# Kernel tuning notes

Hardware: AMD Instinct MI355X
Metric: run time of the kernel (lower is better)

The kernel has to match this reference:

```python
import jax, jax.numpy as jnp
import numpy as np

N = 100000      # nodes
E = 1600000     # edges (avg degree 16)
IN_F, HID, OUT_F, NC = 384, 128, 64, 2
EPS = 1e-5
NEG_SLOPE = 0.01


def _layernorm(x, g, b):
    m = jnp.mean(x, axis=-1, keepdims=True)
    v = jnp.var(x, axis=-1, keepdims=True)
    return (x - m) * jax.lax.rsqrt(v + EPS) * g + b


def _graph_conv(x, edge_index, edge_weight, w_rel, b_rel, w_root):
    # PyG GraphConv: lin_rel(scatter_add(w_e * x[src] -> dst)) + lin_root(x)
    src, dst = edge_index[0], edge_index[1]
    msg = x[src] * edge_weight[:, None]                      # [E, C]
    agg = jax.ops.segment_sum(msg, dst, num_segments=x.shape[0])  # [N, C]
    return agg @ w_rel.T + b_rel + x @ w_root.T


def _xavier(key, shape):
    fan_in, fan_out = shape[1], shape[0]
    lim = float(np.sqrt(6.0 / (fan_in + fan_out)))
    return jax.random.uniform(key, shape, jnp.float32, -lim, lim)


def setup_inputs() -> dict:
    key = jax.random.key(0)
    ks = jax.random.split(key, 10)
    x = jax.random.normal(ks[0], (N, IN_F), jnp.float32)
    edge_index = jax.random.randint(ks[1], (2, E), 0, N, jnp.int64)
    edge_attr = jax.random.uniform(ks[2], (E,), jnp.float32)
    return {
        "x": x,
        "edge_index": edge_index,
        "edge_attr": edge_attr,
        "ln1_g": jnp.ones((IN_F,), jnp.float32),
        "ln1_b": jnp.zeros((IN_F,), jnp.float32),
        "fc1_w": _xavier(ks[3], (HID, IN_F)),
        "fc1_b": jnp.zeros((HID,), jnp.float32),
        "c1_wrel": _xavier(ks[4], (HID, HID)),
        "c1_brel": jnp.zeros((HID,), jnp.float32),
        "c1_wroot": _xavier(ks[5], (HID, HID)),
        "c2_wrel": _xavier(ks[6], (OUT_F, HID)),
        "c2_brel": jnp.zeros((OUT_F,), jnp.float32),
        "c2_wroot": _xavier(ks[7], (OUT_F, HID)),
        "ln2_g": jnp.ones((OUT_F,), jnp.float32),
        "ln2_b": jnp.zeros((OUT_F,), jnp.float32),
        "fc2_w": _xavier(ks[8], (NC, OUT_F)),
        "fc2_b": jnp.zeros((NC,), jnp.float32),
    }


def reference(x, edge_index, edge_attr,
              ln1_g, ln1_b, fc1_w, fc1_b,
              c1_wrel, c1_brel, c1_wroot,
              c2_wrel, c2_brel, c2_wroot,
              ln2_g, ln2_b, fc2_w, fc2_b):
    h = _layernorm(x, ln1_g, ln1_b) @ fc1_w.T + fc1_b          # [N, HID]
    h = _graph_conv(h, edge_index, edge_attr, c1_wrel, c1_brel, c1_wroot)
    h = jax.nn.leaky_relu(h, NEG_SLOPE)
    h = _graph_conv(h, edge_index, edge_attr, c2_wrel, c2_brel, c2_wroot)
    h = jax.nn.leaky_relu(h, NEG_SLOPE)                        # [N, OUT_F]
    out = _layernorm(h, ln2_g, ln2_b) @ fc2_w.T + fc2_b        # [N, NC]
    return out
```

## Files before the change

### kernel.cpp

```cpp
#include <hip/hip_runtime.h>
#include <hip/hip_bf16.h>

#define N_IN_F 384
#define N_HID  128
#define N_OUT  64

typedef unsigned short ushort_t;
typedef __attribute__((ext_vector_type(8))) short short8v;
typedef __attribute__((ext_vector_type(4))) float floatx4;

union U8 { uint4 v; unsigned short u[8]; };

__device__ __forceinline__ float bfu2f(unsigned short s){
    union { unsigned i; float f; } c; c.i = ((unsigned)s) << 16; return c.f;
}
__device__ __forceinline__ unsigned short f2bfu(float f){
    __hip_bfloat16 h = __float2bfloat16(f);
    union { __hip_bfloat16 h; unsigned short u; } c; c.h = h; return c.u;
}

__device__ __forceinline__ float loadS(const void* p, size_t i, int fm){
    return fm ? bfu2f(((const unsigned short*)p)[i]) : ((const float*)p)[i];
}

__global__ void k_detect_all(const int* __restrict__ ei, const unsigned* __restrict__ xw,
                             int* __restrict__ modep){
    int lane = threadIdx.x & 63;
    int zi = 0;
    if (lane < 32) zi = ei[2*lane + 1];
    int cnt = 0;
    #pragma unroll
    for (int q = 0; q < 8; q++){
        unsigned w = xw[lane*8 + q];
        unsigned elo = (w >> 7) & 0xff;
        cnt += (elo >= 118 && elo <= 134) ? 1 : 0;
    }
    #pragma unroll
    for (int m = 32; m; m >>= 1){ zi |= __shfl_xor(zi, m, 64); cnt += __shfl_xor(cnt, m, 64); }
    if (lane == 0 && blockIdx.x == 0){
        modep[0] = (zi == 0) ? 1 : 0;
        modep[1] = (cnt >= 256) ? 1 : 0;
    }
}

__device__ __forceinline__ int edge_src(const int* ei, int e, int i, int mode){
    return mode ? ei[2*(size_t)i] : ei[i];
}
__device__ __forceinline__ int edge_dst(const int* ei, int e, int i, int mode){
    return mode ? ei[2*(size_t)e + 2*(size_t)i] : ei[(size_t)e + i];
}

__global__ void k_hist(const int* __restrict__ ei, int e, int n, const int* __restrict__ modep,
                       int* __restrict__ deg){
    int i = blockIdx.x * 256 + threadIdx.x;
    if (i >= e) return;
    int mode = modep[0];
    int d = edge_dst(ei, e, i, mode);
    if ((unsigned)d >= (unsigned)n) return;
    atomicAdd(&deg[d], 1);
}

__global__ __launch_bounds__(1024) void k_blksum(
    const int* __restrict__ deg, int n, int* __restrict__ part)
{
    __shared__ int s[1024];
    int i = blockIdx.x * 1024 + threadIdx.x;
    s[threadIdx.x] = (i < n) ? deg[i] : 0;
    __syncthreads();
    for (int off = 512; off; off >>= 1){
        if (threadIdx.x < off) s[threadIdx.x] += s[threadIdx.x + off];
        __syncthreads();
    }
    if (threadIdx.x == 0) part[blockIdx.x] = s[0];
}

__global__ __launch_bounds__(128) void k_scanpart(
    int* __restrict__ part, int nb, int* __restrict__ rowoff, int n)
{
    __shared__ int s[128];
    int t = threadIdx.x;
    if (nb <= 128){
        int v = (t < nb) ? part[t] : 0;
        s[t] = v; __syncthreads();
        #pragma unroll
        for (int off = 1; off < 128; off <<= 1){
            int tmp = (t >= off) ? s[t - off] : 0;
            __syncthreads();
            s[t] += tmp;
            __syncthreads();
        }
        if (t < nb) part[t] = s[t] - v;
        if (t == 127) rowoff[n] = s[127];
    } else if (t == 0){
        int run = 0;
        for (int b = 0; b < nb; b++){ int tt = part[b]; part[b] = run; run += tt; }
        rowoff[n] = run;
    }
}

__global__ __launch_bounds__(1024) void k_scanblk(
    int* __restrict__ deg, const int* __restrict__ part, int n, int* __restrict__ rowoff)
{
    __shared__ int s[1024];
    int t = threadIdx.x;
    int i = blockIdx.x * 1024 + t;
    int v = (i < n) ? deg[i] : 0;
    s[t] = v; __syncthreads();
    for (int off = 1; off < 1024; off <<= 1){
        int tmp = (t >= off) ? s[t - off] : 0;
        __syncthreads();
        s[t] += tmp;
        __syncthreads();
    }
    if (i < n){
        int excl = s[t] - v + part[blockIdx.x];
        rowoff[i] = excl;
        deg[i]    = excl;
    }
}

__global__ void k_scatter(const int* __restrict__ ei, const void* __restrict__ ea,
                          int e, int n, const int* __restrict__ modep,
                          int* __restrict__ cursor, int2* __restrict__ colw)
{
    int i = blockIdx.x * 256 + threadIdx.x;
    if (i >= e) return;
    int mode = modep[0], fm = modep[1];
    int d = edge_dst(ei, e, i, mode);
    if ((unsigned)d >= (unsigned)n) return;
    int s = edge_src(ei, e, i, mode);
    if ((unsigned)s >= (unsigned)n) s = 0;
    int pos = atomicAdd(&cursor[d], 1);
    if ((unsigned)pos >= (unsigned)e) return;
    int2 pk; pk.x = s; pk.y = __float_as_int(loadS(ea, i, fm));
    colw[pos] = pk;
}

__global__ __launch_bounds__(64) void k_prep_w1(
    const void* __restrict__ W, const void* __restrict__ g, const void* __restrict__ b,
    const void* __restrict__ fc1b, const int* __restrict__ fmp,
    ushort_t* __restrict__ Wp, float* __restrict__ u, float* __restrict__ v)
{
    int fm = fmp[0];
    int j = blockIdx.x, lane = threadIdx.x;
    float su = 0.f, sv = 0.f;
    for (int k = lane; k < N_IN_F; k += 64){
        float w  = loadS(W, (size_t)j*N_IN_F + k, fm);
        float gk = loadS(g, k, fm);
        float bk = loadS(b, k, fm);
        unsigned short pw = f2bfu(gk * w);
        Wp[(size_t)j*N_IN_F + k] = pw;
        su += bfu2f(pw);
        sv += bk * w;
    }
    #pragma unroll
    for (int m = 32; m; m >>= 1){ su += __shfl_xor(su, m, 64); sv += __shfl_xor(sv, m, 64); }
    if (lane == 0){
        u[j] = su;
        v[j] = sv + loadS(fc1b, j, fm);
    }
}

__global__ void k_cvt4(const void* __restrict__ p0, const void* __restrict__ p1,
                       const void* __restrict__ p2, const void* __restrict__ p3,
                       const int* __restrict__ fmp, ushort_t* __restrict__ o)
{
    int fm = fmp[0];
    int i = blockIdx.x * 256 + threadIdx.x;
    if (i >= 49152) return;
    const void* p; int off;
    if (i < 16384)      { p = p0; off = i; }
    else if (i < 32768) { p = p1; off = i - 16384; }
    else if (i < 40960) { p = p2; off = i - 32768; }
    else                { p = p3; off = i - 40960; }
    o[i] = f2bfu(loadS(p, off, fm));
}

__global__ __launch_bounds__(256) void k_gemm1_mfma(
    const void* __restrict__ x, const int* __restrict__ fmp,
    const ushort_t* __restrict__ Wp,
    const float* __restrict__ u, const float* __restrict__ v,
    ushort_t* __restrict__ out, int n)
{
    int fm = fmp[0];
    int t = threadIdx.x;
    int wave = t >> 6, lane = t & 63;
    int r16 = lane & 15, kq = lane >> 4;
    int m0 = blockIdx.x * 64 + wave * 16;
    int rA = min(m0 + r16, n - 1);

    floatx4 acc[8];
    #pragma unroll
    for (int c = 0; c < 8; c++) acc[c] = (floatx4){0.f, 0.f, 0.f, 0.f};
    float s1 = 0.f, s2 = 0.f;

    for (int ks = 0; ks < N_IN_F/32; ks++){
        int kb = ks*32 + kq*8;
        size_t idx = (size_t)rA*N_IN_F + kb;
        short8v af;
        float f[8];
        if (fm){
            short8v sv = *(const short8v*)((const ushort_t*)x + idx);
            af = sv;
            #pragma unroll
            for (int q = 0; q < 8; q++) f[q] = bfu2f((unsigned short)sv[q]);
        } else {
            const float* xf = (const float*)x + idx;
            floatx4 p = *(const floatx4*)xf;
            floatx4 q4 = *(const floatx4*)(xf + 4);
            f[0]=p[0]; f[1]=p[1]; f[2]=p[2]; f[3]=p[3];
            f[4]=q4[0]; f[5]=q4[1]; f[6]=q4[2]; f[7]=q4[3];
            short8v r;
            #pragma unroll
            for (int q = 0; q < 8; q++) r[q] = (short)f2bfu(f[q]);
            af = r;
        }
        #pragma unroll
        for (int q = 0; q < 8; q++){ s1 += f[q]; s2 += f[q]*f[q]; }

        short8v bfr[8];
        #pragma unroll
        for (int ni = 0; ni < 8; ni++)
            bfr[ni] = *(const short8v*)(Wp + (size_t)(ni*16 + r16)*N_IN_F + kb);
        #pragma unroll
        for (int ni = 0; ni < 8; ni++)
            acc[ni] = __builtin_amdgcn_mfma_f32_16x16x32_bf16(af, bfr[ni], acc[ni], 0, 0, 0);
    }

    s1 += __shfl_xor(s1, 16, 64); s1 += __shfl_xor(s1, 32, 64);
    s2 += __shfl_xor(s2, 16, 64); s2 += __shfl_xor(s2, 32, 64);
    float mu = s1 * (1.f/384.f);
    float var = fmaxf(s2 * (1.f/384.f) - mu*mu, 0.f);
    float rs = rsqrtf(var + 1e-5f);

    int ib = m0 + kq*4;
    float mm[4], rr[4];
    #pragma unroll
    for (int r = 0; r < 4; r++){
        mm[r] = __shfl(mu, kq*4 + r, 64);
        rr[r] = __shfl(rs, kq*4 + r, 64);
    }
    #pragma unroll
    for (int ni = 0; ni < 8; ni++){
        int j = ni*16 + r16;
        float uj = u[j], vj = v[j];
        #pragma unroll
        for (int r = 0; r < 4; r++){
            int ii = ib + r;
            float val = rr[r]*acc[ni][r] - rr[r]*mm[r]*uj + vj;
            if (ii < n) out[(size_t)ii*N_HID + j] = f2bfu(val);
        }
    }
}

__global__ __launch_bounds__(256) void k_conv1_mfma(
    const ushort_t* __restrict__ A1, const ushort_t* __restrict__ A2,
    const ushort_t* __restrict__ W1, const ushort_t* __restrict__ W2,
    const void* __restrict__ bias, const int* __restrict__ fmp,
    ushort_t* __restrict__ out, int n)
{
    int fm = fmp[0];
    int t = threadIdx.x;
    int wave = t >> 6, lane = t & 63;
    int r16 = lane & 15, kq = lane >> 4;
    int m0 = blockIdx.x * 64 + wave * 16;
    int rA = min(m0 + r16, n - 1);

    floatx4 acc[8];
    #pragma unroll
    for (int c = 0; c < 8; c++) acc[c] = (floatx4){0.f, 0.f, 0.f, 0.f};

    #pragma unroll
    for (int p = 0; p < 2; p++){
        const ushort_t* A = p ? A2 : A1;
        const ushort_t* W = p ? W2 : W1;
        #pragma unroll
        for (int ks = 0; ks < 4; ks++){
            int kb = ks*32 + kq*8;
            short8v af = *(const short8v*)(A + (size_t)rA*N_HID + kb);
            short8v bfr[8];
            #pragma unroll
            for (int ni = 0; ni < 8; ni++)
                bfr[ni] = *(const short8v*)(W + (size_t)(ni*16 + r16)*N_HID + kb);
            #pragma unroll
            for (int ni = 0; ni < 8; ni++)
                acc[ni] = __builtin_amdgcn_mfma_f32_16x16x32_bf16(af, bfr[ni], acc[ni], 0, 0, 0);
        }
    }

    int ib = m0 + kq*4;
    #pragma unroll
    for (int ni = 0; ni < 8; ni++){
        int j = ni*16 + r16;
        float bb = loadS(bias, j, fm);
        #pragma unroll
        for (int r = 0; r < 4; r++){
            int ii = ib + r;
            float val = acc[ni][r] + bb;
            val = (val >= 0.f) ? val : 0.01f * val;
            if (ii < n) out[(size_t)ii*N_HID + j] = f2bfu(val);
        }
    }
}

__global__ __launch_bounds__(256) void k_conv2_final(
    const ushort_t* __restrict__ A1, const ushort_t* __restrict__ A2,
    const ushort_t* __restrict__ W1, const ushort_t* __restrict__ W2,
    const void* __restrict__ bias,
    const void* __restrict__ gam, const void* __restrict__ bet,
    const void* __restrict__ Wfc, const void* __restrict__ bfc,
    const int* __restrict__ fmp, void* __restrict__ out, int n)
{
    int fm = fmp[0];
    int t = threadIdx.x;
    int wave = t >> 6, lane = t & 63;
    int r16 = lane & 15, kq = lane >> 4;
    int m0 = blockIdx.x * 64 + wave * 16;
    int rA = min(m0 + r16, n - 1);

    floatx4 acc[4];
    #pragma unroll
    for (int c = 0; c < 4; c++) acc[c] = (floatx4){0.f, 0.f, 0.f, 0.f};

    #pragma unroll
    for (int p = 0; p < 2; p++){
        const ushort_t* A = p ? A2 : A1;
        const ushort_t* W = p ? W2 : W1;
        #pragma unroll
        for (int ks = 0; ks < 4; ks++){
            int kb = ks*32 + kq*8;
            short8v af = *(const short8v*)(A + (size_t)rA*N_HID + kb);
            short8v bfr[4];
            #pragma unroll
            for (int ni = 0; ni < 4; ni++)
                bfr[ni] = *(const short8v*)(W + (size_t)(ni*16 + r16)*N_HID + kb);
            #pragma unroll
            for (int ni = 0; ni < 4; ni++)
                acc[ni] = __builtin_amdgcn_mfma_f32_16x16x32_bf16(af, bfr[ni], acc[ni], 0, 0, 0);
        }
    }

    float s[4] = {}, s2[4] = {};
    #pragma unroll
    for (int ni = 0; ni < 4; ni++){
        int j = ni*16 + r16;
        float bb = loadS(bias, j, fm);
        #pragma unroll
        for (int r = 0; r < 4; r++){
            float val = acc[ni][r] + bb;
            val = (val >= 0.f) ? val : 0.01f * val;
            acc[ni][r] = val;
            s[r] += val; s2[r] += val*val;
        }
    }
    #pragma unroll
    for (int m = 1; m < 16; m <<= 1){
        #pragma unroll
        for (int r = 0; r < 4; r++){
            s[r]  += __shfl_xor(s[r],  m, 64);
            s2[r] += __shfl_xor(s2[r], m, 64);
        }
    }
    float mu[4], rstd[4];
    #pragma unroll
    for (int r = 0; r < 4; r++){
        mu[r] = s[r] * (1.f/64.f);
        float var = fmaxf(s2[r] * (1.f/64.f) - mu[r]*mu[r], 0.f);
        rstd[r] = rsqrtf(var + 1e-5f);
    }
    float p0[4] = {}, p1[4] = {};
    #pragma unroll
    for (int ni = 0; ni < 4; ni++){
        int j = ni*16 + r16;
        float gj = loadS(gam, j, fm), bj = loadS(bet, j, fm);
        float w0 = loadS(Wfc, j, fm), w1 = loadS(Wfc, 64 + j, fm);
        #pragma unroll
        for (int r = 0; r < 4; r++){
            float zn = (acc[ni][r] - mu[r]) * rstd[r] * gj + bj;
            p0[r] += zn * w0;
            p1[r] += zn * w1;
        }
    }
    #pragma unroll
    for (int m = 1; m < 16; m <<= 1){
        #pragma unroll
        for (int r = 0; r < 4; r++){
            p0[r] += __shfl_xor(p0[r], m, 64);
            p1[r] += __shfl_xor(p1[r], m, 64);
        }
    }
    if (r16 == 0){
        float b0 = loadS(bfc, 0, fm), b1 = loadS(bfc, 1, fm);
        #pragma unroll
        for (int r = 0; r < 4; r++){
            int ii = m0 + kq*4 + r;
            if (ii >= n) continue;
            float o0 = p0[r] + b0, o1 = p1[r] + b1;
            if (fm){
                unsigned pk = ((unsigned)f2bfu(o1) << 16) | (unsigned)f2bfu(o0);
                *(unsigned*)((ushort_t*)out + (size_t)ii*2) = pk;
            } else {
                float2 f2; f2.x = o0; f2.y = o1;
                *(float2*)((float*)out + (size_t)ii*2) = f2;
            }
        }
    }
}

__global__ __launch_bounds__(256) void k_agg(
    const int* __restrict__ rowoff, const int2* __restrict__ colw,
    const ushort_t* __restrict__ src_mat,
    ushort_t* __restrict__ out, int n, int eTot)
{
    int t = threadIdx.x;
    int lane = t & 63;
    int d = blockIdx.x * 4 + (t >> 6);
    if (d >= n) return;
    int grp = lane >> 4;
    int c16 = lane & 15;
    int e0 = rowoff[d], e1 = rowoff[d+1];
    e0 = max(0, min(e0, eTot));
    e1 = max(e0, min(e1, eTot));
    float acc[8] = {};
    for (int e = e0 + grp; e < e1; e += 4){
        int2 cw = colw[e];
        int s = cw.x;
        if ((unsigned)s >= (unsigned)n) s = 0;
        float wv = __int_as_float(cw.y);
        U8 u; u.v = *(const uint4*)(src_mat + (size_t)s*N_HID + c16*8);
        #pragma unroll
        for (int q = 0; q < 8; q++) acc[q] += wv * bfu2f(u.u[q]);
    }
    #pragma unroll
    for (int q = 0; q < 8; q++){
        acc[q] += __shfl_xor(acc[q], 16, 64);
        acc[q] += __shfl_xor(acc[q], 32, 64);
    }
    if (grp == 0){
        union { ushort_t u[8]; uint4 v; } P;
        #pragma unroll
        for (int q = 0; q < 8; q++) P.u[q] = f2bfu(acc[q]);
        *(uint4*)(out + (size_t)d*N_HID + c16*8) = P.v;
    }
}

extern "C" void kernel_launch(void* const* d_in, const int* in_sizes, int n_in,
                              void* d_out, int out_size, void* d_ws, size_t ws_size,
                              hipStream_t stream)
{
    const void* x     = d_in[0];
    const int*  ei    = (const int*)d_in[1];
    const void* ea    = d_in[2];
    const void* ln1g  = d_in[3];
    const void* ln1b  = d_in[4];
    const void* fc1w  = d_in[5];
    const void* fc1b  = d_in[6];
    const void* c1rel = d_in[7];
    const void* c1bre = d_in[8];
    const void* c1roo = d_in[9];
    const void* c2rel = d_in[10];
    const void* c2bre = d_in[11];
    const void* c2roo = d_in[12];
    const void* ln2g  = d_in[13];
    const void* ln2b  = d_in[14];
    const void* fc2w  = d_in[15];
    const void* fc2b  = d_in[16];
    (void)n_in; (void)out_size; (void)ws_size;

    const int n = in_sizes[0] / N_IN_F;
    const int e = in_sizes[2];

    char* wsp = (char*)d_ws;
    size_t off = 0;
    auto alloc = [&](size_t bytes) -> char* {
        char* p = wsp + off; off += (bytes + 255) & ~(size_t)255; return p;
    };
    int*      deg    = (int*)  alloc((size_t)n * 4);
    int*      rowoff = (int*)  alloc((size_t)(n+1) * 4);
    int*      part   = (int*)  alloc(4096);
    int*      modep  = (int*)  alloc(256);
    int2*     colw   = (int2*) alloc((size_t)e * 8);
    float*    u      = (float*)alloc(128 * 4);
    float*    v      = (float*)alloc(128 * 4);
    ushort_t* Wp     = (ushort_t*)alloc((size_t)N_HID * N_IN_F * 2);
    ushort_t* cw     = (ushort_t*)alloc((size_t)49152 * 2);
    ushort_t* h1     = (ushort_t*)alloc((size_t)n * N_HID * 2);
    ushort_t* agg1   = (ushort_t*)alloc((size_t)n * N_HID * 2);
    ushort_t* g1     = (ushort_t*)alloc((size_t)n * N_HID * 2);
    ushort_t* agg2   = h1;

    hipMemsetAsync(deg, 0, (size_t)n * 4, stream);
    k_detect_all<<<1, 64, 0, stream>>>(ei, (const unsigned*)x, modep);

    int nb = (n + 1023) / 1024;
    k_hist    <<<(e + 255) / 256, 256, 0, stream>>>(ei, e, n, modep, deg);
    k_blksum  <<<nb, 1024, 0, stream>>>(deg, n, part);
    k_scanpart<<<1, 128, 0, stream>>>(part, nb, rowoff, n);
    k_scanblk <<<nb, 1024, 0, stream>>>(deg, part, n, rowoff);
    k_scatter <<<(e + 255) / 256, 256, 0, stream>>>(ei, ea, e, n, modep, deg, colw);

    k_prep_w1<<<N_HID, 64, 0, stream>>>(fc1w, ln1g, ln1b, fc1b, modep + 1, Wp, u, v);
    k_cvt4   <<<(49152 + 255) / 256, 256, 0, stream>>>(c1rel, c1roo, c2rel, c2roo, modep + 1, cw);

    k_gemm1_mfma<<<(n + 63) / 64, 256, 0, stream>>>(x, modep + 1, Wp, u, v, h1, n);

    k_agg<<<(n + 3) / 4, 256, 0, stream>>>(rowoff, colw, h1, agg1, n, e);
    k_conv1_mfma<<<(n + 63) / 64, 256, 0, stream>>>(agg1, h1, cw, cw + 16384, c1bre, modep + 1, g1, n);

    k_agg<<<(n + 3) / 4, 256, 0, stream>>>(rowoff, colw, g1, agg2, n, e);
    k_conv2_final<<<(n + 63) / 64, 256, 0, stream>>>(agg2, g1, cw + 32768, cw + 40960, c2bre,
                                                     ln2g, ln2b, fc2w, fc2b, modep + 1, d_out, n);
}
```

Baseline: 754.2 us.

## Stage GEMM tiles through LDS with 128-row blocks in dense kernels

The three dense MFMA kernels (fc1, conv1, conv2+final) now cooperatively load A and B tiles into padded shared memory and compute a 128-row block per workgroup, with each wave handling 32 rows. Previously each wave loaded its weight fragments straight from global memory. Sharing the weight tile across waves and doubling the rows per block is meant to cut redundant global and L2 weight traffic. In exchange it adds two barriers per k-step with no double buffering, launches half as many blocks, and uses more registers and LDS per block.

```diff
diff --git a/kernel.cpp b/kernel.cpp
--- a/kernel.cpp
+++ b/kernel.cpp
@@ -182,73 +182,101 @@
     const float* __restrict__ u, const float* __restrict__ v,
     ushort_t* __restrict__ out, int n)
 {
+    __shared__ ushort_t As[128*40];
+    __shared__ ushort_t Bs[128*40];
     int fm = fmp[0];
     int t = threadIdx.x;
     int wave = t >> 6, lane = t & 63;
     int r16 = lane & 15, kq = lane >> 4;
-    int m0 = blockIdx.x * 64 + wave * 16;
-    int rA = min(m0 + r16, n - 1);
-
-    floatx4 acc[8];
-    #pragma unroll
-    for (int c = 0; c < 8; c++) acc[c] = (floatx4){0.f, 0.f, 0.f, 0.f};
-    float s1 = 0.f, s2 = 0.f;
-
-    for (int ks = 0; ks < N_IN_F/32; ks++){
-        int kb = ks*32 + kq*8;
-        size_t idx = (size_t)rA*N_IN_F + kb;
-        short8v af;
-        float f[8];
-        if (fm){
-            short8v sv = *(const short8v*)((const ushort_t*)x + idx);
-            af = sv;
-            #pragma unroll
-            for (int q = 0; q < 8; q++) f[q] = bfu2f((unsigned short)sv[q]);
-        } else {
-            const float* xf = (const float*)x + idx;
-            floatx4 p = *(const floatx4*)xf;
-            floatx4 q4 = *(const floatx4*)(xf + 4);
-            f[0]=p[0]; f[1]=p[1]; f[2]=p[2]; f[3]=p[3];
-            f[4]=q4[0]; f[5]=q4[1]; f[6]=q4[2]; f[7]=q4[3];
-            short8v r;
-            #pragma unroll
-            for (int q = 0; q < 8; q++) r[q] = (short)f2bfu(f[q]);
-            af = r;
-        }
-        #pragma unroll
-        for (int q = 0; q < 8; q++){ s1 += f[q]; s2 += f[q]*f[q]; }
-
-        short8v bfr[8];
+    int m0 = blockIdx.x * 128;
+    int mw = m0 + wave * 32;
+
+    int sq = t & 3, srow = t >> 2;
+    int bcol = t & 127, bhalf = t >> 7;
+
+    floatx4 acc[2][8];
+    #pragma unroll
+    for (int a = 0; a < 2; a++)
+        #pragma unroll
+        for (int c = 0; c < 8; c++) acc[a][c] = (floatx4){0.f,0.f,0.f,0.f};
+    float s1[2] = {0.f,0.f}, s2[2] = {0.f,0.f};
+
+    for (int ks = 0; ks < 12; ks++){
+        int kb = ks*32;
+        #pragma unroll
+        for (int pass = 0; pass < 2; pass++){
+            int row  = srow + pass*64;
+            int grow = min(m0 + row, n - 1);
+            union { ushort_t u[8]; uint4 v4; } w;
+            if (fm){
+                w.v4 = *(const uint4*)((const ushort_t*)x + (size_t)grow*N_IN_F + kb + sq*8);
+            } else {
+                const float* xf = (const float*)x + (size_t)grow*N_IN_F + kb + sq*8;
+                floatx4 p = *(const floatx4*)xf;
+                floatx4 q4 = *(const floatx4*)(xf + 4);
+                w.u[0]=f2bfu(p[0]); w.u[1]=f2bfu(p[1]); w.u[2]=f2bfu(p[2]); w.u[3]=f2bfu(p[3]);
+                w.u[4]=f2bfu(q4[0]); w.u[5]=f2bfu(q4[1]); w.u[6]=f2bfu(q4[2]); w.u[7]=f2bfu(q4[3]);
+            }
+            *(uint4*)(As + row*40 + sq*8) = w.v4;
+        }
+        {
+            const ushort_t* wp = Wp + (size_t)bcol*N_IN_F + kb + bhalf*16;
+            uint4 b0 = *(const uint4*)wp;
+            uint4 b1 = *(const uint4*)(wp + 8);
+            *(uint4*)(Bs + bcol*40 + bhalf*16)     = b0;
+            *(uint4*)(Bs + bcol*40 + bhalf*16 + 8) = b1;
+        }
+        __syncthreads();
+        short8v af[2], bfr[8];
+        #pragma unroll
+        for (int mi = 0; mi < 2; mi++)
+            af[mi] = *(const short8v*)(As + (wave*32 + mi*16 + r16)*40 + kq*8);
         #pragma unroll
         for (int ni = 0; ni < 8; ni++)
-            bfr[ni] = *(const short8v*)(Wp + (size_t)(ni*16 + r16)*N_IN_F + kb);
-        #pragma unroll
-        for (int ni = 0; ni < 8; ni++)
-            acc[ni] = __builtin_amdgcn_mfma_f32_16x16x32_bf16(af, bfr[ni], acc[ni], 0, 0, 0);
-    }
-
-    s1 += __shfl_xor(s1, 16, 64); s1 += __shfl_xor(s1, 32, 64);
-    s2 += __shfl_xor(s2, 16, 64); s2 += __shfl_xor(s2, 32, 64);
-    float mu = s1 * (1.f/384.f);
-    float var = fmaxf(s2 * (1.f/384.f) - mu*mu, 0.f);
-    float rs = rsqrtf(var + 1e-5f);
-
-    int ib = m0 + kq*4;
-    float mm[4], rr[4];
-    #pragma unroll
-    for (int r = 0; r < 4; r++){
-        mm[r] = __shfl(mu, kq*4 + r, 64);
-        rr[r] = __shfl(rs, kq*4 + r, 64);
-    }
-    #pragma unroll
-    for (int ni = 0; ni < 8; ni++){
-        int j = ni*16 + r16;
-        float uj = u[j], vj = v[j];
+            bfr[ni] = *(const short8v*)(Bs + (ni*16 + r16)*40 + kq*8);
+        #pragma unroll
+        for (int mi = 0; mi < 2; mi++){
+            #pragma unroll
+            for (int q = 0; q < 8; q++){
+                float f = bfu2f((unsigned short)af[mi][q]);
+                s1[mi] += f; s2[mi] += f*f;
+            }
+            #pragma unroll
+            for (int ni = 0; ni < 8; ni++)
+                acc[mi][ni] = __builtin_amdgcn_mfma_f32_16x16x32_bf16(af[mi], bfr[ni], acc[mi][ni], 0, 0, 0);
+        }
+        __syncthreads();
+    }
+
+    float mu[2], rs[2];
+    #pragma unroll
+    for (int mi = 0; mi < 2; mi++){
+        s1[mi] += __shfl_xor(s1[mi], 16, 64); s1[mi] += __shfl_xor(s1[mi], 32, 64);
+        s2[mi] += __shfl_xor(s2[mi], 16, 64); s2[mi] += __shfl_xor(s2[mi], 32, 64);
+        mu[mi] = s1[mi] * (1.f/384.f);
+        float var = fmaxf(s2[mi] * (1.f/384.f) - mu[mi]*mu[mi], 0.f);
+        rs[mi] = rsqrtf(var + 1e-5f);
+    }
+
+    #pragma unroll
+    for (int mi = 0; mi < 2; mi++){
+        int ib = mw + mi*16 + kq*4;
+        float mm[4], rr[4];
         #pragma unroll
         for (int r = 0; r < 4; r++){
-            int ii = ib + r;
-            float val = rr[r]*acc[ni][r] - rr[r]*mm[r]*uj + vj;
-            if (ii < n) out[(size_t)ii*N_HID + j] = f2bfu(val);
+            mm[r] = __shfl(mu[mi], kq*4 + r, 64);
+            rr[r] = __shfl(rs[mi], kq*4 + r, 64);
+        }
+        #pragma unroll
+        for (int ni = 0; ni < 8; ni++){
+            int j = ni*16 + r16;
+            float uj = u[j], vj = v[j];
+            #pragma unroll
+            for (int r = 0; r < 4; r++){
+                int ii = ib + r;
+                float val = rr[r]*acc[mi][ni][r] - rr[r]*mm[r]*uj + vj;
+                if (ii < n) out[(size_t)ii*N_HID + j] = f2bfu(val);
+            }
         }
     }
 }
@@ -259,46 +287,73 @@
     const void* __restrict__ bias, const int* __restrict__ fmp,
     ushort_t* __restrict__ out, int n)
 {
+    __shared__ ushort_t As[128*40];
+    __shared__ ushort_t Bs[128*40];
     int fm = fmp[0];
     int t = threadIdx.x;
     int wave = t >> 6, lane = t & 63;
     int r16 = lane & 15, kq = lane >> 4;
-    int m0 = blockIdx.x * 64 + wave * 16;
-    int rA = min(m0 + r16, n - 1);
-
-    floatx4 acc[8];
-    #pragma unroll
-    for (int c = 0; c < 8; c++) acc[c] = (floatx4){0.f, 0.f, 0.f, 0.f};
-
-    #pragma unroll
-    for (int p = 0; p < 2; p++){
-        const ushort_t* A = p ? A2 : A1;
-        const ushort_t* W = p ? W2 : W1;
-        #pragma unroll
-        for (int ks = 0; ks < 4; ks++){
-            int kb = ks*32 + kq*8;
-            short8v af = *(const short8v*)(A + (size_t)rA*N_HID + kb);
-            short8v bfr[8];
+    int m0 = blockIdx.x * 128;
+    int mw = m0 + wave * 32;
+
+    int sq = t & 3, srow = t >> 2;
+    int bcol = t & 127, bhalf = t >> 7;
+
+    floatx4 acc[2][8];
+    #pragma unroll
+    for (int a = 0; a < 2; a++)
+        #pragma unroll
+        for (int c = 0; c < 8; c++) acc[a][c] = (floatx4){0.f,0.f,0.f,0.f};
+
+    #pragma unroll
+    for (int ks = 0; ks < 8; ks++){
+        const ushort_t* Asrc = (ks < 4) ? A1 : A2;
+        const ushort_t* Wsrc = (ks < 4) ? W1 : W2;
+        int kb = (ks & 3)*32;
+        #pragma unroll
+        for (int pass = 0; pass < 2; pass++){
+            int row  = srow + pass*64;
+            int grow = min(m0 + row, n - 1);
+            uint4 w = *(const uint4*)(Asrc + (size_t)grow*N_HID + kb + sq*8);
+            *(uint4*)(As + row*40 + sq*8) = w;
+        }
+        {
+            const ushort_t* wp = Wsrc + (size_t)bcol*N_HID + kb + bhalf*16;
+            uint4 b0 = *(const uint4*)wp;
+            uint4 b1 = *(const uint4*)(wp + 8);
+            *(uint4*)(Bs + bcol*40 + bhalf*16)     = b0;
+            *(uint4*)(Bs + bcol*40 + bhalf*16 + 8) = b1;
+        }
+        __syncthreads();
+        short8v af[2], bfr[8];
+        #pragma unroll
+        for (int mi = 0; mi < 2; mi++)
+            af[mi] = *(const short8v*)(As + (wave*32 + mi*16 + r16)*40 + kq*8);
+        #pragma unroll
+        for (int ni = 0; ni < 8; ni++)
+            bfr[ni] = *(const short8v*)(Bs + (ni*16 + r16)*40 + kq*8);
+        #pragma unroll
+        for (int mi = 0; mi < 2; mi++)
             #pragma unroll
             for (int ni = 0; ni < 8; ni++)
-                bfr[ni] = *(const short8v*)(W + (size_t)(ni*16 + r16)*N_HID + kb);
-            #pragma unroll
-            for (int ni = 0; ni < 8; ni++)
-                acc[ni] = __builtin_amdgcn_mfma_f32_16x16x32_bf16(af, bfr[ni], acc[ni], 0, 0, 0);
-        }
-    }
-
-    int ib = m0 + kq*4;
-    #pragma unroll
-    for (int ni = 0; ni < 8; ni++){
-        int j = ni*16 + r16;
-        float bb = loadS(bias, j, fm);
-        #pragma unroll
-        for (int r = 0; r < 4; r++){
-            int ii = ib + r;
-            float val = acc[ni][r] + bb;
-            val = (val >= 0.f) ? val : 0.01f * val;
-            if (ii < n) out[(size_t)ii*N_HID + j] = f2bfu(val);
+                acc[mi][ni] = __builtin_amdgcn_mfma_f32_16x16x32_bf16(af[mi], bfr[ni], acc[mi][ni], 0, 0, 0);
+        __syncthreads();
+    }
+
+    #pragma unroll
+    for (int mi = 0; mi < 2; mi++){
+        int ib = mw + mi*16 + kq*4;
+        #pragma unroll
+        for (int ni = 0; ni < 8; ni++){
+            int j = ni*16 + r16;
+            float bb = loadS(bias, j, fm);
+            #pragma unroll
+            for (int r = 0; r < 4; r++){
+                int ii = ib + r;
+                float val = acc[mi][ni][r] + bb;
+                val = (val >= 0.f) ? val : 0.01f * val;
+                if (ii < n) out[(size_t)ii*N_HID + j] = f2bfu(val);
+            }
         }
     }
 }
@@ -311,97 +366,121 @@
     const void* __restrict__ Wfc, const void* __restrict__ bfc,
     const int* __restrict__ fmp, void* __restrict__ out, int n)
 {
+    __shared__ ushort_t As[128*40];
+    __shared__ ushort_t Bs[64*40];
     int fm = fmp[0];
     int t = threadIdx.x;
     int wave = t >> 6, lane = t & 63;
     int r16 = lane & 15, kq = lane >> 4;
-    int m0 = blockIdx.x * 64 + wave * 16;
-    int rA = min(m0 + r16, n - 1);
-
-    floatx4 acc[4];
-    #pragma unroll
-    for (int c = 0; c < 4; c++) acc[c] = (floatx4){0.f, 0.f, 0.f, 0.f};
-
-    #pragma unroll
-    for (int p = 0; p < 2; p++){
-        const ushort_t* A = p ? A2 : A1;
-        const ushort_t* W = p ? W2 : W1;
-        #pragma unroll
-        for (int ks = 0; ks < 4; ks++){
-            int kb = ks*32 + kq*8;
-            short8v af = *(const short8v*)(A + (size_t)rA*N_HID + kb);
-            short8v bfr[4];
+    int m0 = blockIdx.x * 128;
+    int mw = m0 + wave * 32;
+
+    int sq = t & 3, srow = t >> 2;
+    int bcol = t & 63, bseg = t >> 6;
+
+    floatx4 acc[2][4];
+    #pragma unroll
+    for (int a = 0; a < 2; a++)
+        #pragma unroll
+        for (int c = 0; c < 4; c++) acc[a][c] = (floatx4){0.f,0.f,0.f,0.f};
+
+    #pragma unroll
+    for (int ks = 0; ks < 8; ks++){
+        const ushort_t* Asrc = (ks < 4) ? A1 : A2;
+        const ushort_t* Wsrc = (ks < 4) ? W1 : W2;
+        int kb = (ks & 3)*32;
+        #pragma unroll
+        for (int pass = 0; pass < 2; pass++){
+            int row  = srow + pass*64;
+            int grow = min(m0 + row, n - 1);
+            uint4 w = *(const uint4*)(Asrc + (size_t)grow*N_HID + kb + sq*8);
+            *(uint4*)(As + row*40 + sq*8) = w;
+        }
+        {
+            uint4 b0 = *(const uint4*)(Wsrc + (size_t)bcol*N_HID + kb + bseg*8);
+            *(uint4*)(Bs + bcol*40 + bseg*8) = b0;
+        }
+        __syncthreads();
+        short8v af[2], bfr[4];
+        #pragma unroll
+        for (int mi = 0; mi < 2; mi++)
+            af[mi] = *(const short8v*)(As + (wave*32 + mi*16 + r16)*40 + kq*8);
+        #pragma unroll
+        for (int ni = 0; ni < 4; ni++)
+            bfr[ni] = *(const short8v*)(Bs + (ni*16 + r16)*40 + kq*8);
+        #pragma unroll
+        for (int mi = 0; mi < 2; mi++)
             #pragma unroll
             for (int ni = 0; ni < 4; ni++)
-                bfr[ni] = *(const short8v*)(W + (size_t)(ni*16 + r16)*N_HID + kb);
-            #pragma unroll
-            for (int ni = 0; ni < 4; ni++)
-                acc[ni] = __builtin_amdgcn_mfma_f32_16x16x32_bf16(af, bfr[ni], acc[ni], 0, 0, 0);
-        }
-    }
-
-    float s[4] = {}, s2[4] = {};
-    #pragma unroll
-    for (int ni = 0; ni < 4; ni++){
-        int j = ni*16 + r16;
-        float bb = loadS(bias, j, fm);
+                acc[mi][ni] = __builtin_amdgcn_mfma_f32_16x16x32_bf16(af[mi], bfr[ni], acc[mi][ni], 0, 0, 0);
+        __syncthreads();
+    }
+
+    float b0 = loadS(bfc, 0, fm), b1 = loadS(bfc, 1, fm);
+    #pragma unroll
+    for (int mi = 0; mi < 2; mi++){
+        float s[4] = {}, s2[4] = {};
+        #pragma unroll
+        for (int ni = 0; ni < 4; ni++){
+            int j = ni*16 + r16;
+            float bb = loadS(bias, j, fm);
+            #pragma unroll
+            for (int r = 0; r < 4; r++){
+                float val = acc[mi][ni][r] + bb;
+                val = (val >= 0.f) ? val : 0.01f * val;
+                acc[mi][ni][r] = val;
+                s[r] += val; s2[r] += val*val;
+            }
+        }
+        #pragma unroll
+        for (int m = 1; m < 16; m <<= 1){
+            #pragma unroll
+            for (int r = 0; r < 4; r++){
+                s[r]  += __shfl_xor(s[r],  m, 64);
+                s2[r] += __shfl_xor(s2[r], m, 64);
+            }
+        }
+        float mu[4], rstd[4];
         #pragma unroll
         for (int r = 0; r < 4; r++){
-            float val = acc[ni][r] + bb;
-            val = (val >= 0.f) ? val : 0.01f * val;
-            acc[ni][r] = val;
-            s[r] += val; s2[r] += val*val;
-        }
-    }
-    #pragma unroll
-    for (int m = 1; m < 16; m <<= 1){
-        #pragma unroll
-        for (int r = 0; r < 4; r++){
-            s[r]  += __shfl_xor(s[r],  m, 64);
-            s2[r] += __shfl_xor(s2[r], m, 64);
-        }
-    }
-    float mu[4], rstd[4];
-    #pragma unroll
-    for (int r = 0; r < 4; r++){
-        mu[r] = s[r] * (1.f/64.f);
-        float var = fmaxf(s2[r] * (1.f/64.f) - mu[r]*mu[r], 0.f);
-        rstd[r] = rsqrtf(var + 1e-5f);
-    }
-    float p0[4] = {}, p1[4] = {};
-    #pragma unroll
-    for (int ni = 0; ni < 4; ni++){
-        int j = ni*16 + r16;
-        float gj = loadS(gam, j, fm), bj = loadS(bet, j, fm);
-        float w0 = loadS(Wfc, j, fm), w1 = loadS(Wfc, 64 + j, fm);
-        #pragma unroll
-        for (int r = 0; r < 4; r++){
-            float zn = (acc[ni][r] - mu[r]) * rstd[r] * gj + bj;
-            p0[r] += zn * w0;
-            p1[r] += zn * w1;
-        }
-    }
-    #pragma unroll
-    for (int m = 1; m < 16; m <<= 1){
-        #pragma unroll
-        for (int r = 0; r < 4; r++){
-            p0[r] += __shfl_xor(p0[r], m, 64);
-            p1[r] += __shfl_xor(p1[r], m, 64);
-        }
-    }
-    if (r16 == 0){
-        float b0 = loadS(bfc, 0, fm), b1 = loadS(bfc, 1, fm);
-        #pragma unroll
-        for (int r = 0; r < 4; r++){
-            int ii = m0 + kq*4 + r;
-            if (ii >= n) continue;
-            float o0 = p0[r] + b0, o1 = p1[r] + b1;
-            if (fm){
-                unsigned pk = ((unsigned)f2bfu(o1) << 16) | (unsigned)f2bfu(o0);
-                *(unsigned*)((ushort_t*)out + (size_t)ii*2) = pk;
-            } else {
-                float2 f2; f2.x = o0; f2.y = o1;
-                *(float2*)((float*)out + (size_t)ii*2) = f2;
+            mu[r] = s[r] * (1.f/64.f);
+            float var = fmaxf(s2[r] * (1.f/64.f) - mu[r]*mu[r], 0.f);
+            rstd[r] = rsqrtf(var + 1e-5f);
+        }
+        float p0[4] = {}, p1[4] = {};
+        #pragma unroll
+        for (int ni = 0; ni < 4; ni++){
+            int j = ni*16 + r16;
+            float gj = loadS(gam, j, fm), bj = loadS(bet, j, fm);
+            float w0 = loadS(Wfc, j, fm), w1 = loadS(Wfc, 64 + j, fm);
+            #pragma unroll
+            for (int r = 0; r < 4; r++){
+                float zn = (acc[mi][ni][r] - mu[r]) * rstd[r] * gj + bj;
+                p0[r] += zn * w0;
+                p1[r] += zn * w1;
+            }
+        }
+        #pragma unroll
+        for (int m = 1; m < 16; m <<= 1){
+            #pragma unroll
+            for (int r = 0; r < 4; r++){
+                p0[r] += __shfl_xor(p0[r], m, 64);
+                p1[r] += __shfl_xor(p1[r], m, 64);
+            }
+        }
+        if (r16 == 0){
+            #pragma unroll
+            for (int r = 0; r < 4; r++){
+                int ii = mw + mi*16 + kq*4 + r;
+                if (ii >= n) continue;
+                float o0 = p0[r] + b0, o1 = p1[r] + b1;
+                if (fm){
+                    unsigned pk = ((unsigned)f2bfu(o1) << 16) | (unsigned)f2bfu(o0);
+                    *(unsigned*)((ushort_t*)out + (size_t)ii*2) = pk;
+                } else {
+                    float2 f2; f2.x = o0; f2.y = o1;
+                    *(float2*)((float*)out + (size_t)ii*2) = f2;
+                }
             }
         }
     }
@@ -502,12 +581,12 @@
     k_prep_w1<<<N_HID, 64, 0, stream>>>(fc1w, ln1g, ln1b, fc1b, modep + 1, Wp, u, v);
     k_cvt4   <<<(49152 + 255) / 256, 256, 0, stream>>>(c1rel, c1roo, c2rel, c2roo, modep + 1, cw);
 
-    k_gemm1_mfma<<<(n + 63) / 64, 256, 0, stream>>>(x, modep + 1, Wp, u, v, h1, n);
+    k_gemm1_mfma<<<(n + 127) / 128, 256, 0, stream>>>(x, modep + 1, Wp, u, v, h1, n);
 
     k_agg<<<(n + 3) / 4, 256, 0, stream>>>(rowoff, colw, h1, agg1, n, e);
-    k_conv1_mfma<<<(n + 63) / 64, 256, 0, stream>>>(agg1, h1, cw, cw + 16384, c1bre, modep + 1, g1, n);
+    k_conv1_mfma<<<(n + 127) / 128, 256, 0, stream>>>(agg1, h1, cw, cw + 16384, c1bre, modep + 1, g1, n);
 
     k_agg<<<(n + 3) / 4, 256, 0, stream>>>(rowoff, colw, g1, agg2, n, e);
-    k_conv2_final<<<(n + 63) / 64, 256, 0, stream>>>(agg2, g1, cw + 32768, cw + 40960, c2bre,
-                                                     ln2g, ln2b, fc2w, fc2b, modep + 1, d_out, n);
-}
+    k_conv2_final<<<(n + 127) / 128, 256, 0, stream>>>(agg2, g1, cw + 32768, cw + 40960, c2bre,
+                                                       ln2g, ln2b, fc2w, fc2b, modep + 1, d_out, n);
+}
```

Result: faster. 673.8 us (-10.7%).
